# Performance work log

Hardware: AMD Instinct MI355X
Metric: run time of the kernel (lower is better)

Reference implementation:

```python
import jax, jax.numpy as jnp
import numpy as np

N = 100000   # total nodes (batched molecules)
E = 250000   # directed edges
B = 2000     # number of graphs
F_IN = 75    # atom feature dim
DIM = 32     # hidden dim


def setup_inputs() -> dict:
    key = jax.random.key(0)
    ks = jax.random.split(key, 12)
    def gl(k, shape, fan_in):
        return (jax.random.normal(k, shape, jnp.float32) / np.sqrt(fan_in)).astype(jnp.float32)
    inp = {}
    inp['node_features'] = jax.random.normal(ks[0], (N, F_IN), jnp.float32)
    inp['edge_features'] = jax.random.normal(ks[1], (E, 11), jnp.float32)
    inp['lin0_w'] = gl(ks[2], (DIM, F_IN), F_IN)
    inp['lin0_b'] = jnp.zeros((DIM,), jnp.float32)
    # edge network: Linear(11,128) -> ReLU -> Linear(128, DIM*DIM)
    inp['nn_w1'] = gl(ks[3], (128, 11), 11)
    inp['nn_b1'] = jnp.zeros((128,), jnp.float32)
    inp['nn_w2'] = gl(ks[4], (DIM * DIM, 128), 128)
    inp['nn_b2'] = jnp.zeros((DIM * DIM,), jnp.float32)
    inp['conv_bias'] = jnp.zeros((DIM,), jnp.float32)  # NNConv bias (root_weight=False)
    # GRU(dim, dim), torch gate order: r, z, n
    inp['gru_wih'] = gl(ks[5], (3 * DIM, DIM), DIM)
    inp['gru_whh'] = gl(ks[6], (3 * DIM, DIM), DIM)
    inp['gru_bih'] = jnp.zeros((3 * DIM,), jnp.float32)
    inp['gru_bhh'] = jnp.zeros((3 * DIM,), jnp.float32)
    # Set2Set LSTM(2*dim, dim), torch gate order: i, f, g, o
    inp['lstm_wih'] = gl(ks[7], (4 * DIM, 2 * DIM), 2 * DIM)
    inp['lstm_whh'] = gl(ks[8], (4 * DIM, DIM), DIM)
    inp['lstm_bih'] = jnp.zeros((4 * DIM,), jnp.float32)
    inp['lstm_bhh'] = jnp.zeros((4 * DIM,), jnp.float32)
    inp['edge_index'] = jax.random.randint(ks[9], (2, E), 0, N)
    inp['graph_index'] = jnp.sort(jax.random.randint(ks[10], (N,), 0, B))
    return inp


def _nnconv(x, edge_w, src, dst, bias):
    # per-edge: gather src features, apply [dim,dim] edge weight, scatter-mean to dst
    msg = jnp.einsum('ei,eio->eo', x[src], edge_w)           # [E, DIM]
    s = jax.ops.segment_sum(msg, dst, num_segments=N)         # [N, DIM]
    cnt = jax.ops.segment_sum(jnp.ones((msg.shape[0],), msg.dtype), dst, num_segments=N)
    mean = s / jnp.maximum(cnt, 1.0)[:, None]
    return mean + bias


def _gru_cell(x, h, wih, whh, bih, bhh):
    gi = x @ wih.T + bih
    gh = h @ whh.T + bhh
    gi_r, gi_z, gi_n = jnp.split(gi, 3, axis=-1)
    gh_r, gh_z, gh_n = jnp.split(gh, 3, axis=-1)
    r = jax.nn.sigmoid(gi_r + gh_r)
    z = jax.nn.sigmoid(gi_z + gh_z)
    n = jnp.tanh(gi_n + r * gh_n)
    return (1.0 - z) * n + z * h


def _lstm_cell(x, h, c, wih, whh, bih, bhh):
    g = x @ wih.T + bih + h @ whh.T + bhh
    i, f, gg, o = jnp.split(g, 4, axis=-1)
    c = jax.nn.sigmoid(f) * c + jax.nn.sigmoid(i) * jnp.tanh(gg)
    h = jax.nn.sigmoid(o) * jnp.tanh(c)
    return h, c


def _set2set(x, batch, wih, whh, bih, bhh, steps=3):
    dim = x.shape[-1]
    h = jnp.zeros((B, dim), x.dtype)
    c = jnp.zeros((B, dim), x.dtype)
    q_star = jnp.zeros((B, 2 * dim), x.dtype)
    for _ in range(steps):
        q, c = _lstm_cell(q_star, h, c, wih, whh, bih, bhh)
        h = q
        e = jnp.sum(x * q[batch], axis=-1)                    # [N]
        emax = jax.ops.segment_max(e, batch, num_segments=B)
        ex = jnp.exp(e - emax[batch])
        denom = jax.ops.segment_sum(ex, batch, num_segments=B)
        a = ex / denom[batch]
        r = jax.ops.segment_sum(a[:, None] * x, batch, num_segments=B)
        q_star = jnp.concatenate([q, r], axis=-1)
    return q_star


def reference(node_features, edge_features, lin0_w, lin0_b, nn_w1, nn_b1, nn_w2, nn_b2,
              conv_bias, gru_wih, gru_whh, gru_bih, gru_bhh,
              lstm_wih, lstm_whh, lstm_bih, lstm_bhh, edge_index, graph_index):
    src, dst = edge_index[0], edge_index[1]
    out = jax.nn.relu(node_features @ lin0_w.T + lin0_b)      # [N, DIM]
    # edge network (edge_features are fixed -> identical every iteration)
    hw = jax.nn.relu(edge_features @ nn_w1.T + nn_b1)
    edge_w = (hw @ nn_w2.T + nn_b2).reshape(-1, DIM, DIM)     # [E, DIM, DIM]
    h = out
    for _ in range(3):
        m = jax.nn.relu(_nnconv(out, edge_w, src, dst, conv_bias))
        h = _gru_cell(m, h, gru_wih, gru_whh, gru_bih, gru_bhh)
        out = h
    pooled = _set2set(out, graph_index, lstm_wih, lstm_whh, lstm_bih, lstm_bhh)
    return pooled, out
```

## Files before the change

kernel.cpp:

```cpp
#include <hip/hip_runtime.h>
#include <stdint.h>

#define N_NODES  100000
#define N_EDGES  250000
#define N_GRAPHS 2000
#define F_IN     75
#define DIM      32
#define H1       128

#define MSG_BLOCKS 977
#define CH        4
#define NSTAGES   33
#define KT_PAD    (CH * NSTAGES)
#define W2F_HALFS (KT_PAD * 1024)

typedef _Float16 v8h __attribute__((ext_vector_type(8)));
typedef float    v4f __attribute__((ext_vector_type(4)));

__device__ __forceinline__ void gld_lds16(const void* g, void* l) {
    __builtin_amdgcn_global_load_lds(
        (const __attribute__((address_space(1))) unsigned int*)g,
        (__attribute__((address_space(3))) unsigned int*)l, 16, 0, 0);
}

__global__ __launch_bounds__(256) void lin0_kernel(
    const float* __restrict__ nf, const float* __restrict__ w,
    const float* __restrict__ b, float* __restrict__ h) {
    __shared__ float wl[DIM * F_IN];
    __shared__ float bl[DIM];
    int t = threadIdx.x;
    for (int i = t; i < DIM * F_IN; i += 256) wl[i] = w[i];
    if (t < DIM) bl[t] = b[t];
    __syncthreads();
    int nl = t >> 5, o = t & 31;
    #pragma unroll
    for (int p = 0; p < 4; ++p) {
        int n = blockIdx.x * 32 + p * 8 + nl;
        if (n >= N_NODES) continue;
        const float* row = nf + (size_t)n * F_IN;
        float acc = bl[o];
        #pragma unroll
        for (int i = 0; i < F_IN; ++i) acc += row[i] * wl[o * F_IN + i];
        h[n * DIM + o] = fmaxf(acc, 0.f);
    }
}

__global__ __launch_bounds__(256) void prep_w2f_kernel(
    const float* __restrict__ w2, const float* __restrict__ b2,
    _Float16* __restrict__ w2f) {
    int id = blockIdx.x * 256 + threadIdx.x;
    if (id >= W2F_HALFS) return;
    int j    = id & 7;
    int lane = (id >> 3) & 63;
    int ng   = (id >> 9) & 1;
    int kt   = id >> 10;
    int lr = lane & 15, q = lane >> 4;
    int c = kt * 32 + q * 8 + j;
    int o = ng * 16 + lr;
    float val = 0.f;
    if (c < 4096)      val = w2[((c >> 7) * 32 + o) * H1 + (c & 127)];
    else if (c < 4128) val = b2[(c - 4096) * 32 + o];
    w2f[id] = (_Float16)val;
}

__global__ __launch_bounds__(256) void hw_kernel(
    const float* __restrict__ ef, const float* __restrict__ w1,
    const float* __restrict__ b1, _Float16* __restrict__ hwf,
    int e_off) {
    __shared__ float wl[H1 * 11];
    __shared__ float bl[H1];
    int t = threadIdx.x;
    for (int i = t; i < H1 * 11; i += 256) wl[i] = w1[i];
    if (t < H1) bl[t] = b1[t];
    __syncthreads();
    int k = t & 127;
    #pragma unroll
    for (int p = 0; p < 16; ++p) {
        int le = blockIdx.x * 32 + p * 2 + (t >> 7);
        int e  = e_off + le;
        float acc = 0.f;
        if (e < N_EDGES) {
            const float* row = ef + (size_t)e * 11;
            acc = bl[k];
            #pragma unroll
            for (int i = 0; i < 11; ++i) acc += row[i] * wl[k * 11 + i];
            acc = fmaxf(acc, 0.f);
        }
        size_t addr = (size_t)(le >> 4) * 2048 + (k >> 3) * 128 + (le & 15) * 8 + (k & 7);
        hwf[addr] = (_Float16)acc;
    }
}

__global__ __launch_bounds__(256) void cnt_kernel(
    const int* __restrict__ dst, float* __restrict__ cnt) {
    int e = blockIdx.x * 256 + threadIdx.x;
    if (e < N_EDGES) atomicAdd(&cnt[dst[e]], 1.0f);
}

__global__ __launch_bounds__(256) void offs_kernel(
    const int* __restrict__ gidx, int* __restrict__ gstart) {
    int n = blockIdx.x * 256 + threadIdx.x;
    if (n >= N_NODES) return;
    int b = gidx[n];
    if (n == 0) {
        for (int bb = 0; bb <= b; ++bb) gstart[bb] = 0;
    } else {
        int a = gidx[n - 1];
        for (int bb = a + 1; bb <= b; ++bb) gstart[bb] = n;
    }
    if (n == N_NODES - 1) {
        for (int bb = b + 1; bb <= N_GRAPHS; ++bb) gstart[bb] = N_NODES;
    }
}

__global__ __launch_bounds__(256) void msg_kernel(
    const _Float16* __restrict__ hwf, const _Float16* __restrict__ w2f,
    const float* __restrict__ x, const int* __restrict__ src,
    const int* __restrict__ dst, float* __restrict__ sbuf, int e_off) {
    __shared__ _Float16 xs[32 * 256];
    __shared__ _Float16 bst[2][CH * 1024];

    int t = threadIdx.x;
    int w = t >> 6, lane = t & 63, lr = lane & 15, q = lane >> 4;
    int wbase = w * 64;

    {
        const char* gp = (const char*)w2f;
        char* lp = (char*)&bst[0][0];
        gld_lds16(gp + t * 16, lp + t * 16);
        gld_lds16(gp + 4096 + t * 16, lp + 4096 + t * 16);
    }

    v8h hwr[4][4];
    {
        const v8h* hv = (const v8h*)hwf;
        int T0 = blockIdx.x * 16 + w * 4;
        #pragma unroll
        for (int mt = 0; mt < 4; ++mt)
            #pragma unroll
            for (int kc = 0; kc < 4; ++kc)
                hwr[mt][kc] = hv[(size_t)(T0 + mt) * 256 + (kc * 4 + q) * 16 + lr];
    }

    {
        int e = e_off + blockIdx.x * 256 + t;
        int ec = e < N_EDGES ? e : N_EDGES - 1;
        int sv = src[ec];
        const float4* xr = (const float4*)(x + (size_t)sv * DIM);
        #pragma unroll
        for (int u = 0; u < 8; ++u) {
            float4 v = xr[u];
            xs[(u * 4 + 0) * 256 + t] = (_Float16)v.x;
            xs[(u * 4 + 1) * 256 + t] = (_Float16)v.y;
            xs[(u * 4 + 2) * 256 + t] = (_Float16)v.z;
            xs[(u * 4 + 3) * 256 + t] = (_Float16)v.w;
        }
    }
    __syncthreads();

    v4f acc[4][2];
    #pragma unroll
    for (int mt = 0; mt < 4; ++mt)
        #pragma unroll
        for (int ng = 0; ng < 2; ++ng) { v4f z = {0.f, 0.f, 0.f, 0.f}; acc[mt][ng] = z; }

    for (int s = 0; s < 32; ++s) {
        {
            const char* gp = (const char*)(w2f + (size_t)(s + 1) * CH * 1024);
            char* lp = (char*)&bst[(s + 1) & 1][0];
            gld_lds16(gp + t * 16, lp + t * 16);
            gld_lds16(gp + 4096 + t * 16, lp + 4096 + t * 16);
        }
        _Float16 xsc[4];
        #pragma unroll
        for (int mt = 0; mt < 4; ++mt)
            xsc[mt] = xs[s * 256 + wbase + mt * 16 + lr];
        const _Float16* bb = &bst[s & 1][0];
        #pragma unroll
        for (int ktl = 0; ktl < CH; ++ktl) {
            v8h b0 = *(const v8h*)(bb + ktl * 1024 + lane * 8);
            v8h b1 = *(const v8h*)(bb + ktl * 1024 + 512 + lane * 8);
            #pragma unroll
            for (int mt = 0; mt < 4; ++mt) {
                v8h a = hwr[mt][ktl] * xsc[mt];
                acc[mt][0] = __builtin_amdgcn_mfma_f32_16x16x32_f16(a, b0, acc[mt][0], 0, 0, 0);
                acc[mt][1] = __builtin_amdgcn_mfma_f32_16x16x32_f16(a, b1, acc[mt][1], 0, 0, 0);
            }
        }
        __syncthreads();
    }
    {
        const _Float16* bb = &bst[0][0];
        v8h b0 = *(const v8h*)(bb + lane * 8);
        v8h b1 = *(const v8h*)(bb + 512 + lane * 8);
        #pragma unroll
        for (int mt = 0; mt < 4; ++mt) {
            v8h a;
            #pragma unroll
            for (int j = 0; j < 8; ++j)
                a[j] = xs[(q * 8 + j) * 256 + wbase + mt * 16 + lr];
            acc[mt][0] = __builtin_amdgcn_mfma_f32_16x16x32_f16(a, b0, acc[mt][0], 0, 0, 0);
            acc[mt][1] = __builtin_amdgcn_mfma_f32_16x16x32_f16(a, b1, acc[mt][1], 0, 0, 0);
        }
    }

    int E0 = e_off + blockIdx.x * 256 + wbase;
    #pragma unroll
    for (int mt = 0; mt < 4; ++mt) {
        #pragma unroll
        for (int r = 0; r < 4; ++r) {
            int e = E0 + mt * 16 + q * 4 + r;
            if (e < N_EDGES) {
                int dv = dst[e];
                float* sp = sbuf + (size_t)dv * DIM;
                atomicAdd(sp + lr,      acc[mt][0][r]);
                atomicAdd(sp + 16 + lr, acc[mt][1][r]);
            }
        }
    }
}

__global__ __launch_bounds__(256) void gru_kernel(
    float* __restrict__ s, const float* __restrict__ cnt,
    const float* __restrict__ cb,
    const float* __restrict__ wih, const float* __restrict__ whh,
    const float* __restrict__ bih, const float* __restrict__ bhh,
    float* __restrict__ h) {
    __shared__ _Float16 wi_l[96 * 40], wh_l[96 * 40];
    __shared__ float bi_l[96], bh_l[96];
    __shared__ _Float16 m_l[64 * 32], h_l[64 * 32];
    int t = threadIdx.x;

    for (int i = t; i < 96 * 32; i += 256) {
        int r = i >> 5, c2 = i & 31;
        wi_l[r * 40 + c2] = (_Float16)wih[i];
        wh_l[r * 40 + c2] = (_Float16)whh[i];
    }
    if (t < 96) { bi_l[t] = bih[t]; bh_l[t] = bhh[t]; }

    {
        int node_l = t >> 2, part = t & 3;
        int n = blockIdx.x * 64 + node_l;
        int nc = n < N_NODES ? n : N_NODES - 1;
        float c = cnt[nc];
        float rc = 1.f / (c > 1.f ? c : 1.f);
        float4* s4 = (float4*)(s + (size_t)nc * DIM + part * 8);
        float4 sa = s4[0], sb = s4[1];
        const float* cbp = cb + part * 8;
        v8h mv;
        mv[0] = (_Float16)fmaxf(sa.x * rc + cbp[0], 0.f);
        mv[1] = (_Float16)fmaxf(sa.y * rc + cbp[1], 0.f);
        mv[2] = (_Float16)fmaxf(sa.z * rc + cbp[2], 0.f);
        mv[3] = (_Float16)fmaxf(sa.w * rc + cbp[3], 0.f);
        mv[4] = (_Float16)fmaxf(sb.x * rc + cbp[4], 0.f);
        mv[5] = (_Float16)fmaxf(sb.y * rc + cbp[5], 0.f);
        mv[6] = (_Float16)fmaxf(sb.z * rc + cbp[6], 0.f);
        mv[7] = (_Float16)fmaxf(sb.w * rc + cbp[7], 0.f);
        *(v8h*)&m_l[node_l * 32 + part * 8] = mv;
        if (n < N_NODES) {
            float4 z4 = {0.f, 0.f, 0.f, 0.f};
            s4[0] = z4; s4[1] = z4;
        }
        const float4* h4 = (const float4*)(h + (size_t)nc * DIM + part * 8);
        float4 ha = h4[0], hb = h4[1];
        v8h hv;
        hv[0] = (_Float16)ha.x; hv[1] = (_Float16)ha.y;
        hv[2] = (_Float16)ha.z; hv[3] = (_Float16)ha.w;
        hv[4] = (_Float16)hb.x; hv[5] = (_Float16)hb.y;
        hv[6] = (_Float16)hb.z; hv[7] = (_Float16)hb.w;
        *(v8h*)&h_l[node_l * 32 + part * 8] = hv;
    }

    __syncthreads();

    int w = t >> 6, lane = t & 63, lr = lane & 15, q = lane >> 4;

    v8h bi6[6], bh6[6];
    v4f ai[6], ah[6];
    #pragma unroll
    for (int nt = 0; nt < 6; ++nt) {
        bi6[nt] = *(const v8h*)&wi_l[(nt * 16 + lr) * 40 + q * 8];
        bh6[nt] = *(const v8h*)&wh_l[(nt * 16 + lr) * 40 + q * 8];
        float bii = bi_l[nt * 16 + lr], bhi = bh_l[nt * 16 + lr];
        v4f ci = {bii, bii, bii, bii}; ai[nt] = ci;
        v4f chh = {bhi, bhi, bhi, bhi}; ah[nt] = chh;
    }

    v8h ma = *(const v8h*)&m_l[(w * 16 + lr) * 32 + q * 8];
    v8h ha = *(const v8h*)&h_l[(w * 16 + lr) * 32 + q * 8];
    #pragma unroll
    for (int nt = 0; nt < 6; ++nt) {
        ai[nt] = __builtin_amdgcn_mfma_f32_16x16x32_f16(ma, bi6[nt], ai[nt], 0, 0, 0);
        ah[nt] = __builtin_amdgcn_mfma_f32_16x16x32_f16(ha, bh6[nt], ah[nt], 0, 0, 0);
    }

    int nb = blockIdx.x * 64 + w * 16 + q * 4;
    #pragma unroll
    for (int g = 0; g < 2; ++g) {
        int o = g * 16 + lr;
        #pragma unroll
        for (int r = 0; r < 4; ++r) {
            int n2 = nb + r;
            if (n2 < N_NODES) {
                float rg = 1.f / (1.f + expf(-(ai[g][r]     + ah[g][r])));
                float zg = 1.f / (1.f + expf(-(ai[2 + g][r] + ah[2 + g][r])));
                float ng = tanhf(ai[4 + g][r] + rg * ah[4 + g][r]);
                float hold = h[(size_t)n2 * DIM + o];
                h[(size_t)n2 * DIM + o] = (1.f - zg) * ng + zg * hold;
            }
        }
    }
}

__global__ __launch_bounds__(256) void s2s_lstm_kernel(
    const float* __restrict__ wih, const float* __restrict__ whh,
    const float* __restrict__ bih, const float* __restrict__ bhh,
    float* __restrict__ h, float* __restrict__ c,
    const float* __restrict__ rnum, const float* __restrict__ denom,
    int first) {
    __shared__ float wA[128 * 33], wB[128 * 33], bl[128];
    int t = threadIdx.x;
    for (int i = t; i < 128 * 32; i += 256) {
        int r = i >> 5, cc = i & 31;
        wA[r * 33 + cc] = wih[r * 64 + cc] + whh[r * 32 + cc];
        wB[r * 33 + cc] = wih[r * 64 + 32 + cc];
    }
    if (t < 128) bl[t] = bih[t] + bhh[t];
    __syncthreads();
    int gl = t >> 5, o = t & 31;
    int b = blockIdx.x * 8 + gl;
    if (b >= N_GRAPHS) return;
    float hq = 0.f, rr = 0.f, cv = 0.f;
    if (!first) {
        hq = h[b * DIM + o];
        float d = denom[b];
        rr = d > 0.f ? rnum[b * DIM + o] / d : 0.f;
        cv = c[b * DIM + o];
    }
    float gi = bl[o], gf = bl[32 + o], gg = bl[64 + o], go = bl[96 + o];
    #pragma unroll
    for (int i = 0; i < 32; ++i) {
        float qv = __shfl(hq, i, 32);
        float rv = __shfl(rr, i, 32);
        gi += qv * wA[o * 33 + i]        + rv * wB[o * 33 + i];
        gf += qv * wA[(32 + o) * 33 + i] + rv * wB[(32 + o) * 33 + i];
        gg += qv * wA[(64 + o) * 33 + i] + rv * wB[(64 + o) * 33 + i];
        go += qv * wA[(96 + o) * 33 + i] + rv * wB[(96 + o) * 33 + i];
    }
    float si = 1.f / (1.f + expf(-gi));
    float sf = 1.f / (1.f + expf(-gf));
    float so = 1.f / (1.f + expf(-go));
    float cn = sf * cv + si * tanhf(gg);
    c[b * DIM + o] = cn;
    h[b * DIM + o] = so * tanhf(cn);
}

__global__ __launch_bounds__(256) void s2s_attn_kernel(
    const float* __restrict__ x, const float* __restrict__ q,
    const int* __restrict__ gstart,
    float* __restrict__ rnum, float* __restrict__ denom,
    float* __restrict__ outp, int wout) {
    int t = threadIdx.x;
    int g = t >> 5, o = t & 31;
    int b = blockIdx.x * 8 + g;
    if (b >= N_GRAPHS) return;
    int n0 = gstart[b], n1 = gstart[b + 1];
    float qo = q[b * DIM + o];
    float m0 = -3.0e38f, s = 0.f, r = 0.f;
    for (int n = n0; n < n1; ++n) {
        float xo = x[(size_t)n * DIM + o];
        float e = xo * qo;
        #pragma unroll
        for (int mm = 16; mm >= 1; mm >>= 1) e += __shfl_xor(e, mm, 32);
        float nm = fmaxf(m0, e);
        float sc = expf(m0 - nm);
        float ex = expf(e - nm);
        s = s * sc + ex;
        r = r * sc + ex * xo;
        m0 = nm;
    }
    rnum[b * DIM + o] = r;
    if (o == 0) denom[b] = s;
    if (wout) {
        outp[b * 64 + o]      = qo;
        outp[b * 64 + 32 + o] = s > 0.f ? r / s : 0.f;
    }
}

extern "C" void kernel_launch(void* const* d_in, const int* in_sizes, int n_in,
                              void* d_out, int out_size, void* d_ws, size_t ws_size,
                              hipStream_t stream) {
    const float* nf   = (const float*)d_in[0];
    const float* ef   = (const float*)d_in[1];
    const float* l0w  = (const float*)d_in[2];
    const float* l0b  = (const float*)d_in[3];
    const float* w1   = (const float*)d_in[4];
    const float* b1   = (const float*)d_in[5];
    const float* w2   = (const float*)d_in[6];
    const float* b2   = (const float*)d_in[7];
    const float* cb   = (const float*)d_in[8];
    const float* gwih = (const float*)d_in[9];
    const float* gwhh = (const float*)d_in[10];
    const float* gbih = (const float*)d_in[11];
    const float* gbhh = (const float*)d_in[12];
    const float* lwih = (const float*)d_in[13];
    const float* lwhh = (const float*)d_in[14];
    const float* lbih = (const float*)d_in[15];
    const float* lbhh = (const float*)d_in[16];
    const int*   eidx = (const int*)d_in[17];
    const int*   gidx = (const int*)d_in[18];
    const int* src = eidx;
    const int* dst = eidx + N_EDGES;
    float* out = (float*)d_out;
    float* h   = out + (size_t)N_GRAPHS * 64;

    char* ws = (char*)d_ws;
    size_t off = 0;
    auto alloc = [&](size_t bytes) -> void* {
        void* p = ws + off;
        off = (off + bytes + 255) & ~(size_t)255;
        return p;
    };
    float* sbuf  = (float*)alloc((size_t)N_NODES * DIM * 4);
    float* cnt   = (float*)alloc((size_t)N_NODES * 4);
    float* hs    = (float*)alloc((size_t)N_GRAPHS * DIM * 4);
    float* cs    = (float*)alloc((size_t)N_GRAPHS * DIM * 4);
    float* rnum  = (float*)alloc((size_t)N_GRAPHS * DIM * 4);
    float* denom = (float*)alloc((size_t)N_GRAPHS * 4);
    int*   gstart = (int*)alloc((size_t)(N_GRAPHS + 1) * 4);
    _Float16* w2f  = (_Float16*)alloc((size_t)W2F_HALFS * 2);
    size_t fixed = off;
    size_t avail = ws_size > fixed ? ws_size - fixed : 0;

    auto need = [&](int nc) -> size_t {
        int cbk = (MSG_BLOCKS + nc - 1) / nc;
        return (size_t)cbk * 16 * 4096;
    };
    int nchunk = 1;
    while (nchunk < 64 && need(nchunk) > avail) nchunk <<= 1;
    int chunk_blocks = (MSG_BLOCKS + nchunk - 1) / nchunk;
    _Float16* hwf = (_Float16*)alloc(need(nchunk));

    lin0_kernel<<<dim3((N_NODES + 31) / 32), dim3(256), 0, stream>>>(nf, l0w, l0b, h);
    prep_w2f_kernel<<<dim3((W2F_HALFS + 255) / 256), dim3(256), 0, stream>>>(w2, b2, w2f);
    hipMemsetAsync(cnt, 0, (size_t)N_NODES * 4, stream);
    cnt_kernel<<<dim3((N_EDGES + 255) / 256), dim3(256), 0, stream>>>(dst, cnt);
    offs_kernel<<<dim3((N_NODES + 255) / 256), dim3(256), 0, stream>>>(gidx, gstart);
    if (nchunk == 1) {
        hw_kernel<<<dim3(MSG_BLOCKS * 8), dim3(256), 0, stream>>>(ef, w1, b1, hwf, 0);
    }
    hipMemsetAsync(sbuf, 0, (size_t)N_NODES * DIM * 4, stream);

    for (int it = 0; it < 3; ++it) {
        for (int cix = 0; cix < nchunk; ++cix) {
            int bstart = cix * chunk_blocks;
            int bc = MSG_BLOCKS - bstart;
            if (bc <= 0) break;
            if (bc > chunk_blocks) bc = chunk_blocks;
            int e_off = bstart * 256;
            if (nchunk > 1)
                hw_kernel<<<dim3(bc * 8), dim3(256), 0, stream>>>(ef, w1, b1, hwf, e_off);
            msg_kernel<<<dim3(bc), dim3(256), 0, stream>>>(hwf, w2f, h, src, dst, sbuf, e_off);
        }
        gru_kernel<<<dim3((N_NODES + 63) / 64), dim3(256), 0, stream>>>(
            sbuf, cnt, cb, gwih, gwhh, gbih, gbhh, h);
    }

    for (int st = 0; st < 3; ++st) {
        s2s_lstm_kernel<<<dim3((N_GRAPHS + 7) / 8), dim3(256), 0, stream>>>(
            lwih, lwhh, lbih, lbhh, hs, cs, rnum, denom, st == 0 ? 1 : 0);
        s2s_attn_kernel<<<dim3((N_GRAPHS + 7) / 8), dim3(256), 0, stream>>>(
            h, hs, gstart, rnum, denom, out, st == 2 ? 1 : 0);
    }
}
```

Baseline: 622.2 us.

## Fuse aux and Set2Set kernels, widen msg pipeline stages, reuse LDS hidden state

Merges the count and graph-offset kernels into one launch and fuses the Set2Set LSTM and attention kernels, which removes launches and a global round-trip of q. Doubles the per-stage chunk of w2f streamed into LDS in msg_kernel (8 k-tiles per stage over 17 stages). That halves the number of barriers but doubles LDS buffer usage, which may reduce occupancy. The GRU now reads the old hidden state from the fp16 LDS copy instead of global memory, which adds a small precision loss.

```diff
diff --git a/kernel.cpp b/kernel.cpp
--- a/kernel.cpp
+++ b/kernel.cpp
@@ -9,10 +9,13 @@
 #define H1       128
 
 #define MSG_BLOCKS 977
-#define CH        4
-#define NSTAGES   33
+#define CH        8
+#define NSTAGES   17
 #define KT_PAD    (CH * NSTAGES)
 #define W2F_HALFS (KT_PAD * 1024)
+
+#define CNT_BLOCKS  ((N_EDGES + 255) / 256)
+#define OFFS_BLOCKS ((N_NODES + 255) / 256)
 
 typedef _Float16 v8h __attribute__((ext_vector_type(8)));
 typedef float    v4f __attribute__((ext_vector_type(4)));
@@ -91,25 +94,26 @@
     }
 }
 
-__global__ __launch_bounds__(256) void cnt_kernel(
-    const int* __restrict__ dst, float* __restrict__ cnt) {
-    int e = blockIdx.x * 256 + threadIdx.x;
-    if (e < N_EDGES) atomicAdd(&cnt[dst[e]], 1.0f);
-}
-
-__global__ __launch_bounds__(256) void offs_kernel(
+__global__ __launch_bounds__(256) void aux_kernel(
+    const int* __restrict__ dst, float* __restrict__ cnt,
     const int* __restrict__ gidx, int* __restrict__ gstart) {
-    int n = blockIdx.x * 256 + threadIdx.x;
-    if (n >= N_NODES) return;
-    int b = gidx[n];
-    if (n == 0) {
-        for (int bb = 0; bb <= b; ++bb) gstart[bb] = 0;
+    int t = threadIdx.x;
+    if (blockIdx.x < CNT_BLOCKS) {
+        int e = blockIdx.x * 256 + t;
+        if (e < N_EDGES) atomicAdd(&cnt[dst[e]], 1.0f);
     } else {
-        int a = gidx[n - 1];
-        for (int bb = a + 1; bb <= b; ++bb) gstart[bb] = n;
-    }
-    if (n == N_NODES - 1) {
-        for (int bb = b + 1; bb <= N_GRAPHS; ++bb) gstart[bb] = N_NODES;
+        int n = (blockIdx.x - CNT_BLOCKS) * 256 + t;
+        if (n >= N_NODES) return;
+        int b = gidx[n];
+        if (n == 0) {
+            for (int bb = 0; bb <= b; ++bb) gstart[bb] = 0;
+        } else {
+            int a = gidx[n - 1];
+            for (int bb = a + 1; bb <= b; ++bb) gstart[bb] = n;
+        }
+        if (n == N_NODES - 1) {
+            for (int bb = b + 1; bb <= N_GRAPHS; ++bb) gstart[bb] = N_NODES;
+        }
     }
 }
 
@@ -127,8 +131,9 @@
     {
         const char* gp = (const char*)w2f;
         char* lp = (char*)&bst[0][0];
-        gld_lds16(gp + t * 16, lp + t * 16);
-        gld_lds16(gp + 4096 + t * 16, lp + 4096 + t * 16);
+        #pragma unroll
+        for (int it = 0; it < 4; ++it)
+            gld_lds16(gp + it * 4096 + t * 16, lp + it * 4096 + t * 16);
     }
 
     v8h hwr[4][4];
@@ -164,25 +169,32 @@
         #pragma unroll
         for (int ng = 0; ng < 2; ++ng) { v4f z = {0.f, 0.f, 0.f, 0.f}; acc[mt][ng] = z; }
 
-    for (int s = 0; s < 32; ++s) {
+    _Float16 xsc[4];
+
+    for (int s = 0; s < NSTAGES - 1; ++s) {
         {
             const char* gp = (const char*)(w2f + (size_t)(s + 1) * CH * 1024);
             char* lp = (char*)&bst[(s + 1) & 1][0];
-            gld_lds16(gp + t * 16, lp + t * 16);
-            gld_lds16(gp + 4096 + t * 16, lp + 4096 + t * 16);
-        }
-        _Float16 xsc[4];
-        #pragma unroll
-        for (int mt = 0; mt < 4; ++mt)
-            xsc[mt] = xs[s * 256 + wbase + mt * 16 + lr];
+            #pragma unroll
+            for (int it = 0; it < 4; ++it)
+                gld_lds16(gp + it * 4096 + t * 16, lp + it * 4096 + t * 16);
+        }
         const _Float16* bb = &bst[s & 1][0];
         #pragma unroll
         for (int ktl = 0; ktl < CH; ++ktl) {
+            int kt = s * CH + ktl;
             v8h b0 = *(const v8h*)(bb + ktl * 1024 + lane * 8);
             v8h b1 = *(const v8h*)(bb + ktl * 1024 + 512 + lane * 8);
+            if ((kt & 3) == 0) {
+                int i = kt >> 2;
+                #pragma unroll
+                for (int mt = 0; mt < 4; ++mt)
+                    xsc[mt] = xs[i * 256 + wbase + mt * 16 + lr];
+            }
+            int kc = kt & 3;
             #pragma unroll
             for (int mt = 0; mt < 4; ++mt) {
-                v8h a = hwr[mt][ktl] * xsc[mt];
+                v8h a = hwr[mt][kc] * xsc[mt];
                 acc[mt][0] = __builtin_amdgcn_mfma_f32_16x16x32_f16(a, b0, acc[mt][0], 0, 0, 0);
                 acc[mt][1] = __builtin_amdgcn_mfma_f32_16x16x32_f16(a, b1, acc[mt][1], 0, 0, 0);
             }
@@ -305,19 +317,20 @@
                 float rg = 1.f / (1.f + expf(-(ai[g][r]     + ah[g][r])));
                 float zg = 1.f / (1.f + expf(-(ai[2 + g][r] + ah[2 + g][r])));
                 float ng = tanhf(ai[4 + g][r] + rg * ah[4 + g][r]);
-                float hold = h[(size_t)n2 * DIM + o];
+                float hold = (float)h_l[(w * 16 + q * 4 + r) * 32 + o];
                 h[(size_t)n2 * DIM + o] = (1.f - zg) * ng + zg * hold;
             }
         }
     }
 }
 
-__global__ __launch_bounds__(256) void s2s_lstm_kernel(
+__global__ __launch_bounds__(256) void s2s_kernel(
     const float* __restrict__ wih, const float* __restrict__ whh,
     const float* __restrict__ bih, const float* __restrict__ bhh,
     float* __restrict__ h, float* __restrict__ c,
-    const float* __restrict__ rnum, const float* __restrict__ denom,
-    int first) {
+    float* __restrict__ rnum, float* __restrict__ denom,
+    const float* __restrict__ x, const int* __restrict__ gstart,
+    float* __restrict__ outp, int first, int wout) {
     __shared__ float wA[128 * 33], wB[128 * 33], bl[128];
     int t = threadIdx.x;
     for (int i = t; i < 128 * 32; i += 256) {
@@ -330,6 +343,7 @@
     int gl = t >> 5, o = t & 31;
     int b = blockIdx.x * 8 + gl;
     if (b >= N_GRAPHS) return;
+
     float hq = 0.f, rr = 0.f, cv = 0.f;
     if (!first) {
         hq = h[b * DIM + o];
@@ -351,21 +365,11 @@
     float sf = 1.f / (1.f + expf(-gf));
     float so = 1.f / (1.f + expf(-go));
     float cn = sf * cv + si * tanhf(gg);
+    float qo = so * tanhf(cn);
     c[b * DIM + o] = cn;
-    h[b * DIM + o] = so * tanhf(cn);
-}
-
-__global__ __launch_bounds__(256) void s2s_attn_kernel(
-    const float* __restrict__ x, const float* __restrict__ q,
-    const int* __restrict__ gstart,
-    float* __restrict__ rnum, float* __restrict__ denom,
-    float* __restrict__ outp, int wout) {
-    int t = threadIdx.x;
-    int g = t >> 5, o = t & 31;
-    int b = blockIdx.x * 8 + g;
-    if (b >= N_GRAPHS) return;
+    h[b * DIM + o] = qo;
+
     int n0 = gstart[b], n1 = gstart[b + 1];
-    float qo = q[b * DIM + o];
     float m0 = -3.0e38f, s = 0.f, r = 0.f;
     for (int n = n0; n < n1; ++n) {
         float xo = x[(size_t)n * DIM + o];
@@ -444,8 +448,7 @@
     lin0_kernel<<<dim3((N_NODES + 31) / 32), dim3(256), 0, stream>>>(nf, l0w, l0b, h);
     prep_w2f_kernel<<<dim3((W2F_HALFS + 255) / 256), dim3(256), 0, stream>>>(w2, b2, w2f);
     hipMemsetAsync(cnt, 0, (size_t)N_NODES * 4, stream);
-    cnt_kernel<<<dim3((N_EDGES + 255) / 256), dim3(256), 0, stream>>>(dst, cnt);
-    offs_kernel<<<dim3((N_NODES + 255) / 256), dim3(256), 0, stream>>>(gidx, gstart);
+    aux_kernel<<<dim3(CNT_BLOCKS + OFFS_BLOCKS), dim3(256), 0, stream>>>(dst, cnt, gidx, gstart);
     if (nchunk == 1) {
         hw_kernel<<<dim3(MSG_BLOCKS * 8), dim3(256), 0, stream>>>(ef, w1, b1, hwf, 0);
     }
@@ -467,9 +470,8 @@
     }
 
     for (int st = 0; st < 3; ++st) {
-        s2s_lstm_kernel<<<dim3((N_GRAPHS + 7) / 8), dim3(256), 0, stream>>>(
-            lwih, lwhh, lbih, lbhh, hs, cs, rnum, denom, st == 0 ? 1 : 0);
-        s2s_attn_kernel<<<dim3((N_GRAPHS + 7) / 8), dim3(256), 0, stream>>>(
-            h, hs, gstart, rnum, denom, out, st == 2 ? 1 : 0);
-    }
-}
+        s2s_kernel<<<dim3((N_GRAPHS + 7) / 8), dim3(256), 0, stream>>>(
+            lwih, lwhh, lbih, lbhh, hs, cs, rnum, denom, h, gstart, out,
+            st == 0 ? 1 : 0, st == 2 ? 1 : 0);
+    }
+}
```

New measurement: 599.5 us. 1.04x faster.
